# Kernel tuning notes

Measured on AMD Instinct MI355X. Metric: run time of the kernel, lower is better.

Reference implementation:

```python
import jax, jax.numpy as jnp
import numpy as np

R_MIN = 0.01
R_MAX = 0.6
H = 32            # polar radial bins (after pooling)
W = 64            # polar angular bins (after pooling)
UP_R = 10         # radial upsampling factor
UP_T = 10         # angular upsampling factor
ATT_ALPHA = 5.0
B, C, IMG = 64, 3, 224


def _conv(x, w, b):
    # NCHW valid conv, stride 1 (matches nn.Conv2d default padding=0)
    y = jax.lax.conv_general_dilated(x, w, (1, 1), 'VALID',
                                     dimension_numbers=('NCHW', 'OIHW', 'NCHW'))
    return y + b[None, :, None, None]


def _maxpool2(x):
    return jax.lax.reduce_window(x, -jnp.inf, jax.lax.max,
                                 (1, 1, 2, 2), (1, 1, 2, 2), 'VALID')


def _grid_sample_border(x, grid):
    # F.grid_sample, bilinear, padding_mode='border', align_corners=False
    Bn, Cn, Hi, Wi = x.shape
    ix = ((grid[..., 0] + 1.0) * Wi - 1.0) * 0.5   # x-coord -> width index
    iy = ((grid[..., 1] + 1.0) * Hi - 1.0) * 0.5   # y-coord -> height index
    x0f = jnp.floor(ix)
    y0f = jnp.floor(iy)
    wx = (ix - x0f)[..., None]
    wy = (iy - y0f)[..., None]
    x0 = jnp.clip(x0f.astype(jnp.int32), 0, Wi - 1)
    x1 = jnp.clip(x0f.astype(jnp.int32) + 1, 0, Wi - 1)
    y0 = jnp.clip(y0f.astype(jnp.int32), 0, Hi - 1)
    y1 = jnp.clip(y0f.astype(jnp.int32) + 1, 0, Hi - 1)
    bidx = jnp.arange(Bn)[:, None, None]
    v00 = x[bidx, :, y0, x0]   # [B,Hg,Wg,C]
    v01 = x[bidx, :, y0, x1]
    v10 = x[bidx, :, y1, x0]
    v11 = x[bidx, :, y1, x1]
    out = (v00 * (1 - wx) * (1 - wy) + v01 * wx * (1 - wy)
           + v10 * (1 - wx) * wy + v11 * wx * wy)
    return jnp.transpose(out, (0, 3, 1, 2))  # [B,C,Hg,Wg]


def setup_inputs() -> dict:
    key = jax.random.key(0)
    ks = jax.random.split(key, 10)
    x = jax.random.normal(ks[0], (B, C, IMG, IMG), dtype=jnp.float32)
    l_t_prev = jax.random.uniform(ks[1], (B, 2), dtype=jnp.float32)
    conv1_w = jax.random.normal(ks[2], (6, C, 5, 5), dtype=jnp.float32) * 0.1
    conv1_b = jnp.zeros((6,), jnp.float32)
    conv2_w = jax.random.normal(ks[3], (16, 6, 5, 5), dtype=jnp.float32) * 0.1
    conv2_b = jnp.zeros((16,), jnp.float32)
    fc1_w = jax.random.normal(ks[4], (8, 16), dtype=jnp.float32) * 0.1
    fc1_b = jnp.zeros((8,), jnp.float32)
    fc2_w = jax.random.normal(ks[5], (2, 8), dtype=jnp.float32) * 0.1
    fc2_b = jnp.zeros((2,), jnp.float32)
    return dict(x=x, l_t_prev=l_t_prev, conv1_w=conv1_w, conv1_b=conv1_b,
                conv2_w=conv2_w, conv2_b=conv2_b, fc1_w=fc1_w, fc1_b=fc1_b,
                fc2_w=fc2_w, fc2_b=fc2_b)


def reference(x, l_t_prev, conv1_w, conv1_b, conv2_w, conv2_b,
              fc1_w, fc1_b, fc2_w, fc2_b):
    # --- attention branch: conv -> maxpool -> conv -> GAP -> fc -> sigmoid ---
    h = _conv(x, conv1_w, conv1_b)
    h = _maxpool2(h)
    h = _conv(h, conv2_w, conv2_b)
    feat = h.mean(axis=(2, 3))                     # AdaptiveAvgPool2d(1), [B,16]
    h = jax.nn.relu(feat @ fc1_w.T + fc1_b)
    weight = jax.nn.sigmoid(h @ fc2_w.T + fc2_b) * ATT_ALPHA   # [B,2]
    # --- per-batch log-polar grid ---
    Hg, Wg = H * UP_R, W * UP_T
    angle = 2.0 * jnp.pi * jnp.arange(Wg, dtype=jnp.float32) / Wg
    unit = jnp.stack([jnp.sin(angle), jnp.cos(angle)], axis=-1)   # [Wg,2]
    start = jnp.log(R_MIN * weight[:, 0])
    stop = jnp.log(R_MAX * weight[:, 1])
    t = jnp.arange(Hg, dtype=jnp.float32) / (Hg - 1)
    radii = jnp.exp(start[:, None] + (stop - start)[:, None] * t[None])  # [B,Hg]
    grid = radii[:, :, None, None] * unit[None, None]     # [B,Hg,Wg,2]
    grid = grid + l_t_prev[:, None, None, :]
    # --- irregular bilinear sampling + box filter ---
    sampled = _grid_sample_border(x, grid)                 # [B,C,Hg,Wg]
    Bn, Cn = sampled.shape[:2]
    pooled = sampled.reshape(Bn, Cn, H, UP_R, W, UP_T).mean(axis=(3, 5))
    return pooled, weight
```

## Files before the change

### kernel.cpp

```cpp
#include <hip/hip_runtime.h>
#include <math.h>

#define Bn    64
#define Cn    3
#define IMG   224
#define PLANE (IMG*IMG)
#define C1    6
#define P1    110
#define P2    106
#define NVALID (P2*P2)
#define Hh    32
#define Ww    64
#define UPR   10
#define UPT   10
#define Hg    (Hh*UPR)
#define Wg    (Ww*UPT)
#define POOLED_SIZE (Bn*Cn*Hh*Ww)
#define RPB   8
#define SROWS (2*RPB+2)

typedef unsigned short u16;

#define WSUM_FLOATS (Bn*C1*25 + Bn*2)
#define X4B_U16     ((size_t)Bn * PLANE * 4)
#define WS_NEEDED   ((size_t)WSUM_FLOATS * 4 + X4B_U16 * 2)

__device__ __forceinline__ u16 f2bf(float f) {
    union { unsigned int u; float f; } c; c.f = f;
    unsigned int r = c.u + 0x7fffu + ((c.u >> 16) & 1u);
    return (u16)(r >> 16);
}
__device__ __forceinline__ float bf2f(u16 v) {
    union { unsigned int u; float f; } c; c.u = ((unsigned int)v) << 16;
    return c.f;
}

__global__ __launch_bounds__(512) void k1_fused(
    const float* __restrict__ x,
    const float* __restrict__ w1,
    const float* __restrict__ b1,
    float* __restrict__ wsum,
    u16* __restrict__ x4b,
    int do_pack)
{
    __shared__ __attribute__((aligned(16))) float xs[3][SROWS][224];

    const int b    = blockIdx.y;
    const int y0   = blockIdx.x * RPB;
    const int tid  = threadIdx.x;
    const int wid  = tid >> 6;
    const int lane = tid & 63;

    const float* xb = x + (size_t)b * (Cn * PLANE);
    const int gybase = 2 * y0;

    #pragma unroll
    for (int it = 0; it < 6; ++it) {
        const int i = tid + it * 512;
        if (i < 3 * SROWS * 56) {
            const int ic  = i / (SROWS * 56);
            const int rem = i - ic * (SROWS * 56);
            const int r   = rem / 56;
            const int c4  = rem - r * 56;
            const int gy  = gybase + r;
            if (gy < IMG)
                *(float4*)(&xs[ic][r][c4 * 4]) =
                    *(const float4*)(xb + ic * PLANE + gy * IMG + c4 * 4);
        }
    }
    __syncthreads();

    if (do_pack) {
        u16* ob = x4b + (size_t)b * PLANE * 4;
        #pragma unroll
        for (int it = 0; it < 7; ++it) {
            const int i   = tid + it * 512;
            const int r   = i / IMG;
            const int col = i - r * IMG;
            const int gy  = gybase + r;
            ushort4 v;
            v.x = f2bf(xs[0][r][col]);
            v.y = f2bf(xs[1][r][col]);
            v.z = f2bf(xs[2][r][col]);
            v.w = 0;
            *(ushort4*)(ob + ((size_t)gy * IMG + col) * 4) = v;
        }
    }

    const int y = y0 + wid;
    const bool rowvalid = (y < P1);
    const bool active = (lane < 55) && rowvalid;

    float pp0[C1], pp1[C1];
    if (active) {
        float acc[C1][8];
        #pragma unroll
        for (int oc = 0; oc < C1; ++oc) {
            const float bv = b1[oc];
            #pragma unroll
            for (int j = 0; j < 8; ++j) acc[oc][j] = bv;
        }

        #pragma unroll
        for (int ic = 0; ic < 3; ++ic) {
            float rTop[8], rBot[8];
            {
                const float* rp = &xs[ic][2 * wid][4 * lane];
                const float4 a = *(const float4*)rp;
                const float4 c = *(const float4*)(rp + 4);
                rTop[0]=a.x; rTop[1]=a.y; rTop[2]=a.z; rTop[3]=a.w;
                rTop[4]=c.x; rTop[5]=c.y; rTop[6]=c.z; rTop[7]=c.w;
            }
            {
                const float* rp = &xs[ic][2 * wid + 1][4 * lane];
                const float4 a = *(const float4*)rp;
                const float4 c = *(const float4*)(rp + 4);
                rBot[0]=a.x; rBot[1]=a.y; rBot[2]=a.z; rBot[3]=a.w;
                rBot[4]=c.x; rBot[5]=c.y; rBot[6]=c.z; rBot[7]=c.w;
            }
            #pragma unroll
            for (int ky = 0; ky < 5; ++ky) {
                #pragma unroll
                for (int oc = 0; oc < C1; ++oc) {
                    const float* wrow = w1 + ((oc * 3 + ic) * 25 + ky * 5);
                    #pragma unroll
                    for (int kx = 0; kx < 5; ++kx) {
                        const float wv = wrow[kx];
                        acc[oc][0] += rTop[kx    ] * wv;
                        acc[oc][1] += rTop[kx + 1] * wv;
                        acc[oc][2] += rTop[kx + 2] * wv;
                        acc[oc][3] += rTop[kx + 3] * wv;
                        acc[oc][4] += rBot[kx    ] * wv;
                        acc[oc][5] += rBot[kx + 1] * wv;
                        acc[oc][6] += rBot[kx + 2] * wv;
                        acc[oc][7] += rBot[kx + 3] * wv;
                    }
                }
                if (ky < 4) {
                    #pragma unroll
                    for (int j = 0; j < 8; ++j) rTop[j] = rBot[j];
                    const float* rp = &xs[ic][2 * wid + ky + 2][4 * lane];
                    const float4 a = *(const float4*)rp;
                    const float4 c = *(const float4*)(rp + 4);
                    rBot[0]=a.x; rBot[1]=a.y; rBot[2]=a.z; rBot[3]=a.w;
                    rBot[4]=c.x; rBot[5]=c.y; rBot[6]=c.z; rBot[7]=c.w;
                }
            }
        }

        #pragma unroll
        for (int oc = 0; oc < C1; ++oc) {
            pp0[oc] = fmaxf(fmaxf(acc[oc][0], acc[oc][1]),
                            fmaxf(acc[oc][4], acc[oc][5]));
            pp1[oc] = fmaxf(fmaxf(acc[oc][2], acc[oc][3]),
                            fmaxf(acc[oc][6], acc[oc][7]));
        }
    } else {
        #pragma unroll
        for (int oc = 0; oc < C1; ++oc) { pp0[oc] = 0.0f; pp1[oc] = 0.0f; }
    }

    #pragma unroll
    for (int oc = 0; oc < C1; ++oc) {
        float s = pp0[oc] + pp1[oc];
        #pragma unroll
        for (int off = 32; off > 0; off >>= 1) s += __shfl_xor(s, off, 64);
        const float c0   = __shfl(pp0[oc], 0, 64);
        const float c1   = __shfl(pp1[oc], 0, 64);
        const float c2   = __shfl(pp0[oc], 1, 64);
        const float c3   = __shfl(pp1[oc], 1, 64);
        const float c106 = __shfl(pp0[oc], 53, 64);
        const float c107 = __shfl(pp1[oc], 53, 64);
        const float c108 = __shfl(pp0[oc], 54, 64);
        const float c109 = __shfl(pp1[oc], 54, 64);
        const float w0v = s - (c106 + c107 + c108 + c109);
        const float w1v = s - c0 - (c107 + c108 + c109);
        const float w2v = s - (c0 + c1) - (c108 + c109);
        const float w3v = s - (c0 + c1 + c2) - c109;
        const float w4v = s - (c0 + c1 + c2 + c3);
        if (rowvalid && lane < 25) {
            const int ky = lane / 5;
            const int kx = lane % 5;
            if ((unsigned)(y - ky) <= 105u) {
                float wv = w0v;
                wv = (kx == 1) ? w1v : wv;
                wv = (kx == 2) ? w2v : wv;
                wv = (kx == 3) ? w3v : wv;
                wv = (kx == 4) ? w4v : wv;
                atomicAdd(wsum + ((size_t)b * C1 + oc) * 25 + lane, wv);
            }
        }
    }
}

__global__ __launch_bounds__(64) void k2_head(
    const float* __restrict__ wsum, const float* __restrict__ w2,
    const float* __restrict__ b2, const float* __restrict__ fc1w,
    const float* __restrict__ fc1b, const float* __restrict__ fc2w,
    const float* __restrict__ fc2b, float* __restrict__ wt_ws,
    float* __restrict__ out)
{
    const int b = blockIdx.x;
    const int tid = threadIdx.x;
    __shared__ float sfeat[16];
    __shared__ float sh[8];

    const float* wsb = wsum + b * 150;
    if (tid < 16) {
        float s = 0.0f;
        for (int j = 0; j < 150; ++j) s += w2[tid * 150 + j] * wsb[j];
        sfeat[tid] = b2[tid] + s * (1.0f / (float)NVALID);
    }
    __syncthreads();
    if (tid < 8) {
        float s = fc1b[tid];
        #pragma unroll
        for (int j = 0; j < 16; ++j) s += fc1w[tid * 16 + j] * sfeat[j];
        sh[tid] = fmaxf(s, 0.0f);
    }
    __syncthreads();
    if (tid < 2) {
        float s = fc2b[tid];
        #pragma unroll
        for (int j = 0; j < 8; ++j) s += fc2w[tid * 8 + j] * sh[j];
        float sig = (s >= 0.0f) ? (1.0f / (1.0f + expf(-s)))
                                : (expf(s) / (1.0f + expf(s)));
        const float wgt = 5.0f * sig;
        wt_ws[b * 2 + tid] = wgt;
        out[POOLED_SIZE + b * 2 + tid] = wgt;
    }
}

__device__ __forceinline__ void sample_coords(
    float gxn, float gyn, int& x0, int& y0, float& wx, float& wy)
{
    float ix = ((gxn + 1.0f) * (float)IMG - 1.0f) * 0.5f;
    float iy = ((gyn + 1.0f) * (float)IMG - 1.0f) * 0.5f;
    ix = fminf(fmaxf(ix, 0.0f), (float)(IMG - 1));
    iy = fminf(fmaxf(iy, 0.0f), (float)(IMG - 1));
    x0 = (int)ix; if (x0 > IMG - 2) x0 = IMG - 2;
    y0 = (int)iy; if (y0 > IMG - 2) y0 = IMG - 2;
    wx = ix - (float)x0;
    wy = iy - (float)y0;
}

__global__ __launch_bounds__(640) void k3_sample_pool_bf16(
    const u16* __restrict__ x4b,
    const float* __restrict__ ltp,
    const float* __restrict__ wt,
    float* __restrict__ out)
{
    __shared__ float part[3 * Wg];

    const int L = blockIdx.x;
    const int q = L >> 3;
    const int h = q & 31;
    const int b = (L & 7) + 8 * (q >> 5);
    const int tid = threadIdx.x;

    const float w0 = wt[b * 2 + 0];
    const float w1 = wt[b * 2 + 1];
    const float l0 = ltp[b * 2 + 0];
    const float l1 = ltp[b * 2 + 1];
    const float start = logf(0.01f * w0);
    const float stop  = logf(0.6f  * w1);
    const float dr = stop - start;

    const float angle = 6.283185307179586f * (float)tid / (float)Wg;
    const float sn = sinf(angle);
    const float cs = cosf(angle);

    const u16* xb4 = x4b + (size_t)b * PLANE * 4;

    const float ratio = expf(dr * (1.0f / (float)(Hg - 1)));
    float r = expf(start + dr * ((float)(h * UPR) / (float)(Hg - 1)));

    float acc0 = 0.0f, acc1 = 0.0f, acc2 = 0.0f;
    #pragma unroll
    for (int i = 0; i < UPR; ++i) {
        int x0, y0; float wx, wy;
        sample_coords(r * sn + l0, r * cs + l1, x0, y0, wx, wy);
        r *= ratio;

        const u16* base = xb4 + ((size_t)(y0 * IMG + x0)) * 4;
        const ushort4 a00 = *(const ushort4*)(base);
        const ushort4 a01 = *(const ushort4*)(base + 4);
        const ushort4 a10 = *(const ushort4*)(base + IMG * 4);
        const ushort4 a11 = *(const ushort4*)(base + IMG * 4 + 4);

        const float wx0 = 1.0f - wx, wy0 = 1.0f - wy;
        const float w00 = wx0 * wy0, w01 = wx * wy0;
        const float w10 = wx0 * wy,  w11 = wx * wy;

        acc0 += w00*bf2f(a00.x) + w01*bf2f(a01.x) + w10*bf2f(a10.x) + w11*bf2f(a11.x);
        acc1 += w00*bf2f(a00.y) + w01*bf2f(a01.y) + w10*bf2f(a10.y) + w11*bf2f(a11.y);
        acc2 += w00*bf2f(a00.z) + w01*bf2f(a01.z) + w10*bf2f(a10.z) + w11*bf2f(a11.z);
    }
    part[0 * Wg + tid] = acc0;
    part[1 * Wg + tid] = acc1;
    part[2 * Wg + tid] = acc2;
    __syncthreads();

    if (tid < Cn * Ww) {
        const int c = tid / Ww;
        const int w = tid % Ww;
        const float* p = part + c * Wg + w * UPT;
        float s = 0.0f;
        #pragma unroll
        for (int j = 0; j < UPT; ++j) s += p[j];
        out[(((size_t)b * Cn + c) * Hh + h) * Ww + w] = s * (1.0f / (UPR * UPT));
    }
}

__global__ __launch_bounds__(640) void k3_sample_pool_nchw(
    const float* __restrict__ x, const float* __restrict__ ltp,
    const float* __restrict__ wt, float* __restrict__ out)
{
    __shared__ float part[3 * Wg];
    const int L = blockIdx.x;
    const int q = L >> 3;
    const int h = q & 31;
    const int b = (L & 7) + 8 * (q >> 5);
    const int tid = threadIdx.x;

    const float w0 = wt[b * 2 + 0];
    const float w1 = wt[b * 2 + 1];
    const float l0 = ltp[b * 2 + 0];
    const float l1 = ltp[b * 2 + 1];
    const float start = logf(0.01f * w0);
    const float stop  = logf(0.6f  * w1);
    const float dr = stop - start;
    const float angle = 6.283185307179586f * (float)tid / (float)Wg;
    const float sn = sinf(angle);
    const float cs = cosf(angle);
    const float* xb = x + (size_t)b * Cn * PLANE;

    const float ratio = expf(dr * (1.0f / (float)(Hg - 1)));
    float r = expf(start + dr * ((float)(h * UPR) / (float)(Hg - 1)));

    float acc0 = 0.0f, acc1 = 0.0f, acc2 = 0.0f;
    #pragma unroll
    for (int i = 0; i < UPR; ++i) {
        int x0, y0; float wx, wy;
        sample_coords(r * sn + l0, r * cs + l1, x0, y0, wx, wy);
        r *= ratio;
        const float wx0 = 1.0f - wx, wy0 = 1.0f - wy;
        const float w00 = wx0 * wy0, w01 = wx * wy0;
        const float w10 = wx0 * wy,  w11 = wx * wy;
        const int o00 = y0 * IMG + x0;
        acc0 += w00*xb[o00] + w01*xb[o00+1] + w10*xb[o00+IMG] + w11*xb[o00+IMG+1];
        const float* x1p = xb + PLANE;
        acc1 += w00*x1p[o00] + w01*x1p[o00+1] + w10*x1p[o00+IMG] + w11*x1p[o00+IMG+1];
        const float* x2p = xb + 2 * PLANE;
        acc2 += w00*x2p[o00] + w01*x2p[o00+1] + w10*x2p[o00+IMG] + w11*x2p[o00+IMG+1];
    }
    part[0 * Wg + tid] = acc0;
    part[1 * Wg + tid] = acc1;
    part[2 * Wg + tid] = acc2;
    __syncthreads();

    if (tid < Cn * Ww) {
        const int c = tid / Ww;
        const int w = tid % Ww;
        const float* p = part + c * Wg + w * UPT;
        float s = 0.0f;
        #pragma unroll
        for (int j = 0; j < UPT; ++j) s += p[j];
        out[(((size_t)b * Cn + c) * Hh + h) * Ww + w] = s * (1.0f / (UPR * UPT));
    }
}

extern "C" void kernel_launch(void* const* d_in, const int* in_sizes, int n_in,
                              void* d_out, int out_size, void* d_ws, size_t ws_size,
                              hipStream_t stream) {
    const float* x       = (const float*)d_in[0];
    const float* ltp     = (const float*)d_in[1];
    const float* conv1_w = (const float*)d_in[2];
    const float* conv1_b = (const float*)d_in[3];
    const float* conv2_w = (const float*)d_in[4];
    const float* conv2_b = (const float*)d_in[5];
    const float* fc1_w   = (const float*)d_in[6];
    const float* fc1_b   = (const float*)d_in[7];
    const float* fc2_w   = (const float*)d_in[8];
    const float* fc2_b   = (const float*)d_in[9];
    float* out = (float*)d_out;

    const int do_pack = (ws_size >= WS_NEEDED) ? 1 : 0;

    float* wsum  = (float*)d_ws;
    float* wt_ws = wsum + Bn * C1 * 25;
    u16*   x4b   = (u16*)(wt_ws + Bn * 2);

    hipMemsetAsync(d_ws, 0, (size_t)WSUM_FLOATS * sizeof(float), stream);

    k1_fused<<<dim3((P1 + RPB - 1) / RPB, Bn), dim3(512), 0, stream>>>(
        x, conv1_w, conv1_b, wsum, x4b, do_pack);
    k2_head<<<dim3(Bn), dim3(64), 0, stream>>>(wsum, conv2_w, conv2_b,
                                               fc1_w, fc1_b, fc2_w, fc2_b,
                                               wt_ws, out);
    if (do_pack)
        k3_sample_pool_bf16<<<dim3(Hh * Bn), dim3(Wg), 0, stream>>>(x4b, ltp, wt_ws, out);
    else
        k3_sample_pool_nchw<<<dim3(Hh * Bn), dim3(Wg), 0, stream>>>(x, ltp, wt_ws, out);
}
```

Baseline: 200.6 us.

## Replace atomic wsum accumulation with per-chunk partials reduced in head kernel

The conv1 kernel now works on 4 pooled rows per block with 256 threads, reduces its per-wave kernel-weight sums in shared memory, and writes one partial vector per chunk instead of using global atomicAdds. The head kernel sums these partials over chunks, which removes the memset launch and the atomic contention. Blocks double in count and each loads a 12-row halo for 4 output rows, so more input is re-read from global memory per block.

```diff
diff --git a/kernel.cpp b/kernel.cpp
--- a/kernel.cpp
+++ b/kernel.cpp
@@ -16,14 +16,15 @@
 #define Hg    (Hh*UPR)
 #define Wg    (Ww*UPT)
 #define POOLED_SIZE (Bn*Cn*Hh*Ww)
-#define RPB   8
-#define SROWS (2*RPB+2)
+#define RPB   4
+#define NCHUNK ((P1 + RPB - 1) / RPB)
+#define PSTRIDE 152
 
 typedef unsigned short u16;
 
-#define WSUM_FLOATS (Bn*C1*25 + Bn*2)
+#define PART_FLOATS ((size_t)Bn * NCHUNK * PSTRIDE)
 #define X4B_U16     ((size_t)Bn * PLANE * 4)
-#define WS_NEEDED   ((size_t)WSUM_FLOATS * 4 + X4B_U16 * 2)
+#define WS_NEEDED   ((PART_FLOATS + Bn * 2) * 4 + X4B_U16 * 2)
 
 __device__ __forceinline__ u16 f2bf(float f) {
     union { unsigned int u; float f; } c; c.f = f;
@@ -35,18 +36,20 @@
     return c.f;
 }
 
-__global__ __launch_bounds__(512) void k1_fused(
+__global__ __launch_bounds__(256) void k1_fused(
     const float* __restrict__ x,
     const float* __restrict__ w1,
     const float* __restrict__ b1,
-    float* __restrict__ wsum,
+    float* __restrict__ partial,
     u16* __restrict__ x4b,
     int do_pack)
 {
-    __shared__ __attribute__((aligned(16))) float xs[3][SROWS][224];
+    __shared__ __attribute__((aligned(16))) float xs[3][12][224];
+    __shared__ float psum[RPB][PSTRIDE];
 
     const int b    = blockIdx.y;
-    const int y0   = blockIdx.x * RPB;
+    const int chunk = blockIdx.x;
+    const int y0   = chunk * RPB;
     const int tid  = threadIdx.x;
     const int wid  = tid >> 6;
     const int lane = tid & 63;
@@ -54,27 +57,21 @@
     const float* xb = x + (size_t)b * (Cn * PLANE);
     const int gybase = 2 * y0;
 
-    #pragma unroll
-    for (int it = 0; it < 6; ++it) {
-        const int i = tid + it * 512;
-        if (i < 3 * SROWS * 56) {
-            const int ic  = i / (SROWS * 56);
-            const int rem = i - ic * (SROWS * 56);
-            const int r   = rem / 56;
-            const int c4  = rem - r * 56;
-            const int gy  = gybase + r;
-            if (gy < IMG)
-                *(float4*)(&xs[ic][r][c4 * 4]) =
-                    *(const float4*)(xb + ic * PLANE + gy * IMG + c4 * 4);
-        }
+    for (int i = tid; i < 3 * 12 * 56; i += 256) {
+        const int ic  = i / (12 * 56);
+        const int rem = i - ic * (12 * 56);
+        const int r   = rem / 56;
+        const int c4  = rem - r * 56;
+        const int gy  = gybase + r;
+        if (gy < IMG)
+            *(float4*)(&xs[ic][r][c4 * 4]) =
+                *(const float4*)(xb + ic * PLANE + gy * IMG + c4 * 4);
     }
     __syncthreads();
 
     if (do_pack) {
         u16* ob = x4b + (size_t)b * PLANE * 4;
-        #pragma unroll
-        for (int it = 0; it < 7; ++it) {
-            const int i   = tid + it * 512;
+        for (int i = tid; i < 8 * IMG; i += 256) {
             const int r   = i / IMG;
             const int col = i - r * IMG;
             const int gy  = gybase + r;
@@ -178,23 +175,28 @@
         const float w2v = s - (c0 + c1) - (c108 + c109);
         const float w3v = s - (c0 + c1 + c2) - c109;
         const float w4v = s - (c0 + c1 + c2 + c3);
-        if (rowvalid && lane < 25) {
+        if (lane < 25) {
             const int ky = lane / 5;
             const int kx = lane % 5;
-            if ((unsigned)(y - ky) <= 105u) {
-                float wv = w0v;
-                wv = (kx == 1) ? w1v : wv;
-                wv = (kx == 2) ? w2v : wv;
-                wv = (kx == 3) ? w3v : wv;
-                wv = (kx == 4) ? w4v : wv;
-                atomicAdd(wsum + ((size_t)b * C1 + oc) * 25 + lane, wv);
-            }
+            float wv = w0v;
+            wv = (kx == 1) ? w1v : wv;
+            wv = (kx == 2) ? w2v : wv;
+            wv = (kx == 3) ? w3v : wv;
+            wv = (kx == 4) ? w4v : wv;
+            const bool valid = rowvalid && ((unsigned)(y - ky) <= 105u);
+            psum[wid][oc * 25 + lane] = valid ? wv : 0.0f;
         }
     }
-}
-
-__global__ __launch_bounds__(64) void k2_head(
-    const float* __restrict__ wsum, const float* __restrict__ w2,
+    __syncthreads();
+
+    if (tid < 150) {
+        const float v = psum[0][tid] + psum[1][tid] + psum[2][tid] + psum[3][tid];
+        partial[((size_t)b * NCHUNK + chunk) * PSTRIDE + tid] = v;
+    }
+}
+
+__global__ __launch_bounds__(256) void k2_head(
+    const float* __restrict__ partial, const float* __restrict__ w2,
     const float* __restrict__ b2, const float* __restrict__ fc1w,
     const float* __restrict__ fc1b, const float* __restrict__ fc2w,
     const float* __restrict__ fc2b, float* __restrict__ wt_ws,
@@ -202,10 +204,18 @@
 {
     const int b = blockIdx.x;
     const int tid = threadIdx.x;
+    __shared__ float wsb[150];
     __shared__ float sfeat[16];
     __shared__ float sh[8];
 
-    const float* wsb = wsum + b * 150;
+    if (tid < 150) {
+        const float* p = partial + (size_t)b * NCHUNK * PSTRIDE + tid;
+        float s = 0.0f;
+        #pragma unroll
+        for (int c = 0; c < NCHUNK; ++c) s += p[c * PSTRIDE];
+        wsb[tid] = s;
+    }
+    __syncthreads();
     if (tid < 16) {
         float s = 0.0f;
         for (int j = 0; j < 150; ++j) s += w2[tid * 150 + j] * wsb[j];
@@ -387,17 +397,15 @@
 
     const int do_pack = (ws_size >= WS_NEEDED) ? 1 : 0;
 
-    float* wsum  = (float*)d_ws;
-    float* wt_ws = wsum + Bn * C1 * 25;
-    u16*   x4b   = (u16*)(wt_ws + Bn * 2);
-
-    hipMemsetAsync(d_ws, 0, (size_t)WSUM_FLOATS * sizeof(float), stream);
-
-    k1_fused<<<dim3((P1 + RPB - 1) / RPB, Bn), dim3(512), 0, stream>>>(
-        x, conv1_w, conv1_b, wsum, x4b, do_pack);
-    k2_head<<<dim3(Bn), dim3(64), 0, stream>>>(wsum, conv2_w, conv2_b,
-                                               fc1_w, fc1_b, fc2_w, fc2_b,
-                                               wt_ws, out);
+    float* part_ws = (float*)d_ws;
+    float* wt_ws   = part_ws + PART_FLOATS;
+    u16*   x4b     = (u16*)(wt_ws + Bn * 2);
+
+    k1_fused<<<dim3(NCHUNK, Bn), dim3(256), 0, stream>>>(
+        x, conv1_w, conv1_b, part_ws, x4b, do_pack);
+    k2_head<<<dim3(Bn), dim3(256), 0, stream>>>(part_ws, conv2_w, conv2_b,
+                                                fc1_w, fc1_b, fc2_w, fc2_b,
+                                                wt_ws, out);
     if (do_pack)
         k3_sample_pool_bf16<<<dim3(Hh * Bn), dim3(Wg), 0, stream>>>(x4b, ltp, wt_ws, out);
     else
```

After: 184.4 us. 8.1% less time.
